# Kernel tuning notes

Hardware: AMD Instinct MI355X
Metric: run time of the kernel (lower is better)

Reference implementation:

```python
import jax, jax.numpy as jnp
import numpy as np

NH = 4096
OBS = 4096
OUT = 4096
T = 16


def _rk4_last(f, h0, t):
    """Fixed-step RK4 odeint over grid t; returns state at t[-1]."""
    def step(h, ts):
        t0, t1 = ts
        dt = t1 - t0
        half = dt * 0.5
        k1 = f(t0, h)
        k2 = f(t0 + half, h + half * k1)
        k3 = f(t0 + half, h + half * k2)
        k4 = f(t1, h + dt * k3)
        return h + (dt / 6.0) * (k1 + 2.0 * k2 + 2.0 * k3 + k4), None
    hT, _ = jax.lax.scan(step, h0, (t[:-1], t[1:]))
    return hT


def setup_inputs() -> dict:
    key = jax.random.key(0)
    ks = jax.random.split(key, 12)
    s = 0.02
    return {
        "x_f": jax.random.normal(ks[0], (1, OBS), jnp.float32),
        "x_b": jax.random.normal(ks[1], (1, OBS), jnp.float32),
        "h_f": jax.random.normal(ks[2], (NH,), jnp.float32),
        "h_b": jax.random.normal(ks[3], (NH,), jnp.float32),
        "t_f": jnp.linspace(0.0, 1.0, T, dtype=jnp.float32),
        "t_b": jnp.linspace(1.0, 0.0, T, dtype=jnp.float32),
        "i2h_W": jax.random.normal(ks[4], (NH, OBS + NH), jnp.float32) * s,
        "i2h_b": jax.random.normal(ks[5], (NH,), jnp.float32) * s,
        "h2o_W": jax.random.normal(ks[6], (OUT, 2 * NH), jnp.float32) * s,
        "h2o_b": jax.random.normal(ks[7], (OUT,), jnp.float32) * s,
        "f_W1": jax.random.normal(ks[8], (NH, NH), jnp.float32) * s,
        "f_b1": jax.random.normal(ks[9], (NH,), jnp.float32) * s,
        "f_W2": jax.random.normal(ks[10], (NH, NH), jnp.float32) * s,
        "f_b2": jax.random.normal(ks[11], (NH,), jnp.float32) * s,
    }


def reference(x_f, x_b, h_f, h_b, t_f, t_b,
              i2h_W, i2h_b, h2o_W, h2o_b, f_W1, f_b1, f_W2, f_b2):
    def func(t, h):  # ODE dynamics: 2-layer tanh MLP (time-independent)
        return f_W2 @ jnp.tanh(f_W1 @ h + f_b1) + f_b2

    def i2h(v):
        return i2h_W @ v + i2h_b

    def gru_update(x, h):
        # NOTE: original computes z and r from the SAME linear on the same
        # input, so z == r; we keep that math faithfully.
        g = jax.nn.sigmoid(i2h(jnp.concatenate([x, h])))
        z, r = g, g
        h_hat = jnp.tanh(i2h(jnp.concatenate([x, r * h])))
        return z * h + (1.0 - z) * h_hat

    h_f = _rk4_last(func, h_f, t_f)
    h_b = _rk4_last(func, h_b, t_b)

    h_f = gru_update(x_f[0], h_f)  # x_f.squeeze(0)
    h_b = gru_update(x_b[0], h_b)

    out = h2o_W @ jnp.concatenate([h_f, h_b]) + h2o_b
    return out, h_f, h_b
```

## Files before the change

kernel.cpp:

```cpp
#include <hip/hip_runtime.h>
#include <math.h>

#define NH   4096
#define KCAT 8192
#define TPTS 16

typedef unsigned short ushort_t;

__device__ __forceinline__ float wave_reduce64(float s) {
#pragma unroll
    for (int off = 32; off > 0; off >>= 1)
        s += __shfl_down(s, off, 64);
    return s;
}

__device__ __forceinline__ unsigned f2bf_pack2(float lo, float hi) {
    unsigned ul = __float_as_uint(lo);
    unsigned uh = __float_as_uint(hi);
    ul = (ul + 0x7fffu + ((ul >> 16) & 1u)) >> 16;
    uh = (uh + 0x7fffu + ((uh >> 16) & 1u)) >> 16;
    return ul | (uh << 16);
}

__device__ __forceinline__ ushort_t bf16_1(float x) {
    unsigned u = __float_as_uint(x);
    return (ushort_t)((u + 0x7fffu + ((u >> 16) & 1u)) >> 16);
}

__device__ __forceinline__ void bf16x8_to_f32(uint4 w, float* f) {
    f[0] = __uint_as_float(w.x << 16); f[1] = __uint_as_float(w.x & 0xffff0000u);
    f[2] = __uint_as_float(w.y << 16); f[3] = __uint_as_float(w.y & 0xffff0000u);
    f[4] = __uint_as_float(w.z << 16); f[5] = __uint_as_float(w.z & 0xffff0000u);
    f[6] = __uint_as_float(w.w << 16); f[7] = __uint_as_float(w.w & 0xffff0000u);
}

__global__ __launch_bounds__(256) void cvt_bf16_kernel(const float* __restrict__ src,
                                                       ushort_t* __restrict__ dst, int n8) {
    int i = blockIdx.x * 256 + threadIdx.x;
    if (i < n8) {
        const float4* s4 = (const float4*)src;
        float4 a = s4[2 * i], b = s4[2 * i + 1];
        uint4 o;
        o.x = f2bf_pack2(a.x, a.y);
        o.y = f2bf_pack2(a.z, a.w);
        o.z = f2bf_pack2(b.x, b.y);
        o.w = f2bf_pack2(b.z, b.w);
        ((uint4*)dst)[i] = o;
    }
}

__global__ __launch_bounds__(256) void init_hu(const float* __restrict__ h_f,
                                               const float* __restrict__ h_b,
                                               float* __restrict__ H,
                                               ushort_t* __restrict__ Ubf) {
    int i = blockIdx.x * 256 + threadIdx.x;
    float a = h_f[i], b = h_b[i];
    H[i]       = a;  H[NH + i]   = b;
    Ubf[i]     = bf16_1(a);
    Ubf[NH + i] = bf16_1(b);
}


__global__ __launch_bounds__(512, 4) void ode_mv1(
    const ushort_t* __restrict__ W1b, const float* __restrict__ b1,
    const ushort_t* __restrict__ Ubf, ushort_t* __restrict__ Vbf)
{
    __shared__ uint4 uS[1024];
    const int t = threadIdx.x;
    {
        const uint4* U4 = (const uint4*)Ubf;
        uS[t]       = U4[t];
        uS[t + 512] = U4[t + 512];
    }
    __syncthreads();

    const int l   = t & 63;
    const int row = blockIdx.x * 8 + (t >> 6);
    const uint4* __restrict__ W4 = (const uint4*)(W1b + (size_t)row * NH);

    float s0 = 0.f, s1 = 0.f;
#pragma unroll
    for (int i = 0; i < 8; ++i) {
        int idx = l + 64 * i;
        uint4 wv = W4[idx];
        uint4 u0 = uS[idx];
        uint4 u1 = uS[512 + idx];
        float wf[8], a0[8], a1[8];
        bf16x8_to_f32(wv, wf);
        bf16x8_to_f32(u0, a0);
        bf16x8_to_f32(u1, a1);
#pragma unroll
        for (int k = 0; k < 8; ++k) {
            s0 += wf[k] * a0[k];
            s1 += wf[k] * a1[k];
        }
    }
    s0 = wave_reduce64(s0);
    s1 = wave_reduce64(s1);
    if (l == 0) {
        float bb = b1[row];
        Vbf[row]      = bf16_1(tanhf(s0 + bb));
        Vbf[NH + row] = bf16_1(tanhf(s1 + bb));
    }
}

__global__ __launch_bounds__(512, 4) void ode_mv2(
    const ushort_t* __restrict__ W2b, const float* __restrict__ b2,
    const ushort_t* __restrict__ Vbf,
    const float* __restrict__ tf, const float* __restrict__ tb, int sidx,
    float wgt, float cnext, int stage,
    float* __restrict__ H, float* __restrict__ ACC,
    ushort_t* __restrict__ Ubf)
{
    __shared__ uint4 vS[1024];
    const int t = threadIdx.x;
    {
        const uint4* V4 = (const uint4*)Vbf;
        vS[t]       = V4[t];
        vS[t + 512] = V4[t + 512];
    }
    __syncthreads();

    const int l   = t & 63;
    const int row = blockIdx.x * 8 + (t >> 6);
    const uint4* __restrict__ W4 = (const uint4*)(W2b + (size_t)row * NH);
    const float dt0 = tf[sidx + 1] - tf[sidx];
    const float dt1 = tb[sidx + 1] - tb[sidx];

    float s0 = 0.f, s1 = 0.f;
#pragma unroll
    for (int i = 0; i < 8; ++i) {
        int idx = l + 64 * i;
        uint4 wv = W4[idx];
        uint4 v0 = vS[idx];
        uint4 v1 = vS[512 + idx];
        float wf[8], a0[8], a1[8];
        bf16x8_to_f32(wv, wf);
        bf16x8_to_f32(v0, a0);
        bf16x8_to_f32(v1, a1);
#pragma unroll
        for (int k = 0; k < 8; ++k) {
            s0 += wf[k] * a0[k];
            s1 += wf[k] * a1[k];
        }
    }
    s0 = wave_reduce64(s0);
    s1 = wave_reduce64(s1);
    if (l == 0) {
        float bb = b2[row];
        float k0 = s0 + bb, k1 = s1 + bb;
        float base0 = (stage == 0) ? H[row]      : ACC[row];
        float base1 = (stage == 0) ? H[NH + row] : ACC[NH + row];
        float a0 = base0 + wgt * (dt0 / 6.f) * k0;
        float a1 = base1 + wgt * (dt1 / 6.f) * k1;
        ACC[row]      = a0;
        ACC[NH + row] = a1;
        if (stage == 3) {
            H[row]      = a0;
            H[NH + row] = a1;
            Ubf[row]      = bf16_1(a0);
            Ubf[NH + row] = bf16_1(a1);
        } else {
            Ubf[row]      = bf16_1(H[row]      + cnext * dt0 * k0);
            Ubf[NH + row] = bf16_1(H[NH + row] + cnext * dt1 * k1);
        }
    }
}

__global__ __launch_bounds__(256) void init_h_kernel(const float* __restrict__ h_f,
                                                     const float* __restrict__ h_b,
                                                     float* __restrict__ H) {
    int i = blockIdx.x * 256 + threadIdx.x;
    H[i]      = h_f[i];
    H[NH + i] = h_b[i];
}

__global__ __launch_bounds__(256) void rk4_mv1_f32(
    const float* __restrict__ W1, const float* __restrict__ b1,
    const float* __restrict__ H,  const float* __restrict__ Kv,
    const float* __restrict__ tf, const float* __restrict__ tb,
    int tidx, float coef, int useK,
    float* __restrict__ V)
{
    const int row  = blockIdx.x * 4 + (threadIdx.x >> 6);
    const int lane = threadIdx.x & 63;
    const float a0 = coef * (tf[tidx + 1] - tf[tidx]);
    const float a1 = coef * (tb[tidx + 1] - tb[tidx]);

    const float4* __restrict__ W4 = (const float4*)(W1 + (size_t)row * NH);
    const float4* __restrict__ x0 = (const float4*)(H);
    const float4* __restrict__ x1 = (const float4*)(H + NH);
    const float4* __restrict__ k0 = (const float4*)(Kv);
    const float4* __restrict__ k1 = (const float4*)(Kv + NH);

    float s0 = 0.f, s1 = 0.f;
    if (useK) {
#pragma unroll 8
        for (int i = 0; i < NH / 4 / 64; ++i) {
            int idx = lane + i * 64;
            float4 w  = W4[idx];
            float4 h0 = x0[idx], h1 = x1[idx];
            float4 p0 = k0[idx], p1 = k1[idx];
            s0 += w.x * (h0.x + a0 * p0.x) + w.y * (h0.y + a0 * p0.y)
                + w.z * (h0.z + a0 * p0.z) + w.w * (h0.w + a0 * p0.w);
            s1 += w.x * (h1.x + a1 * p1.x) + w.y * (h1.y + a1 * p1.y)
                + w.z * (h1.z + a1 * p1.z) + w.w * (h1.w + a1 * p1.w);
        }
    } else {
#pragma unroll 8
        for (int i = 0; i < NH / 4 / 64; ++i) {
            int idx = lane + i * 64;
            float4 w  = W4[idx];
            float4 h0 = x0[idx], h1 = x1[idx];
            s0 += w.x * h0.x + w.y * h0.y + w.z * h0.z + w.w * h0.w;
            s1 += w.x * h1.x + w.y * h1.y + w.z * h1.z + w.w * h1.w;
        }
    }
    s0 = wave_reduce64(s0);
    s1 = wave_reduce64(s1);
    if (lane == 0) {
        float bb = b1[row];
        V[row]      = tanhf(s0 + bb);
        V[NH + row] = tanhf(s1 + bb);
    }
}

__global__ __launch_bounds__(256) void rk4_mv2_f32(
    const float* __restrict__ W2, const float* __restrict__ b2,
    const float* __restrict__ V,
    const float* __restrict__ tf, const float* __restrict__ tb,
    int tidx, float wgt,
    const float* __restrict__ Hbase,
    float* __restrict__ Kout, float* __restrict__ ACC)
{
    const int row  = blockIdx.x * 4 + (threadIdx.x >> 6);
    const int lane = threadIdx.x & 63;

    const float4* __restrict__ W4 = (const float4*)(W2 + (size_t)row * NH);
    const float4* __restrict__ v0 = (const float4*)(V);
    const float4* __restrict__ v1 = (const float4*)(V + NH);

    float s0 = 0.f, s1 = 0.f;
#pragma unroll 8
    for (int i = 0; i < NH / 4 / 64; ++i) {
        int idx = lane + i * 64;
        float4 w = W4[idx];
        float4 a = v0[idx], b = v1[idx];
        s0 += w.x * a.x + w.y * a.y + w.z * a.z + w.w * a.w;
        s1 += w.x * b.x + w.y * b.y + w.z * b.z + w.w * b.w;
    }
    s0 = wave_reduce64(s0);
    s1 = wave_reduce64(s1);
    if (lane == 0) {
        float bb  = b2[row];
        float k0v = s0 + bb;
        float k1v = s1 + bb;
        Kout[row]      = k0v;
        Kout[NH + row] = k1v;
        const float dt0 = tf[tidx + 1] - tf[tidx];
        const float dt1 = tb[tidx + 1] - tb[tidx];
        ACC[row]      = Hbase[row]      + wgt * (dt0 / 6.f) * k0v;
        ACC[NH + row] = Hbase[NH + row] + wgt * (dt1 / 6.f) * k1v;
    }
}

__global__ __launch_bounds__(256) void build_xcat_kernel(
    const float* __restrict__ x_f, const float* __restrict__ x_b,
    const float* __restrict__ H,
    float* __restrict__ xcat1, float* __restrict__ xcat2)
{
    int i = blockIdx.x * 256 + threadIdx.x;
    float xf = x_f[i], xb = x_b[i];
    xcat1[i]               = xf;
    xcat2[i]               = xf;
    xcat1[KCAT + i]        = xb;
    xcat2[KCAT + i]        = xb;
    xcat1[NH + i]          = H[i];
    xcat1[KCAT + NH + i]   = H[NH + i];
}

__global__ __launch_bounds__(256) void gru_mv1(
    const float* __restrict__ Wi, const float* __restrict__ bi,
    const float* __restrict__ xcat1, const float* __restrict__ H,
    float* __restrict__ G, float* __restrict__ xcat2)
{
    const int row  = blockIdx.x * 4 + (threadIdx.x >> 6);
    const int lane = threadIdx.x & 63;

    const float4* __restrict__ W4 = (const float4*)(Wi + (size_t)row * KCAT);
    const float4* __restrict__ c0 = (const float4*)(xcat1);
    const float4* __restrict__ c1 = (const float4*)(xcat1 + KCAT);

    float s0 = 0.f, s1 = 0.f;
#pragma unroll 8
    for (int i = 0; i < KCAT / 4 / 64; ++i) {
        int idx = lane + i * 64;
        float4 w = W4[idx];
        float4 a = c0[idx], b = c1[idx];
        s0 += w.x * a.x + w.y * a.y + w.z * a.z + w.w * a.w;
        s1 += w.x * b.x + w.y * b.y + w.z * b.z + w.w * b.w;
    }
    s0 = wave_reduce64(s0);
    s1 = wave_reduce64(s1);
    if (lane == 0) {
        float bb = bi[row];
        float g0 = 1.f / (1.f + expf(-(s0 + bb)));
        float g1 = 1.f / (1.f + expf(-(s1 + bb)));
        G[row]      = g0;
        G[NH + row] = g1;
        xcat2[NH + row]        = g0 * H[row];
        xcat2[KCAT + NH + row] = g1 * H[NH + row];
    }
}

__global__ __launch_bounds__(256) void gru_mv2(
    const float* __restrict__ Wi, const float* __restrict__ bi,
    const float* __restrict__ xcat2, const float* __restrict__ H,
    const float* __restrict__ G,
    float* __restrict__ out, float* __restrict__ hcat)
{
    const int row  = blockIdx.x * 4 + (threadIdx.x >> 6);
    const int lane = threadIdx.x & 63;

    const float4* __restrict__ W4 = (const float4*)(Wi + (size_t)row * KCAT);
    const float4* __restrict__ c0 = (const float4*)(xcat2);
    const float4* __restrict__ c1 = (const float4*)(xcat2 + KCAT);

    float s0 = 0.f, s1 = 0.f;
#pragma unroll 8
    for (int i = 0; i < KCAT / 4 / 64; ++i) {
        int idx = lane + i * 64;
        float4 w = W4[idx];
        float4 a = c0[idx], b = c1[idx];
        s0 += w.x * a.x + w.y * a.y + w.z * a.z + w.w * a.w;
        s1 += w.x * b.x + w.y * b.y + w.z * b.z + w.w * b.w;
    }
    s0 = wave_reduce64(s0);
    s1 = wave_reduce64(s1);
    if (lane == 0) {
        float bb  = bi[row];
        float hh0 = tanhf(s0 + bb);
        float hh1 = tanhf(s1 + bb);
        float g0  = G[row], g1 = G[NH + row];
        float hf  = g0 * H[row]      + (1.f - g0) * hh0;
        float hb  = g1 * H[NH + row] + (1.f - g1) * hh1;
        out[NH + row]     = hf;
        out[2 * NH + row] = hb;
        hcat[row]      = hf;
        hcat[NH + row] = hb;
    }
}

__global__ __launch_bounds__(256) void h2o_mv(
    const float* __restrict__ W, const float* __restrict__ b,
    const float* __restrict__ hcat, float* __restrict__ out)
{
    const int row  = blockIdx.x * 4 + (threadIdx.x >> 6);
    const int lane = threadIdx.x & 63;

    const float4* __restrict__ W4 = (const float4*)(W + (size_t)row * KCAT);
    const float4* __restrict__ x4 = (const float4*)(hcat);

    float s = 0.f;
#pragma unroll 8
    for (int i = 0; i < KCAT / 4 / 64; ++i) {
        int idx = lane + i * 64;
        float4 w = W4[idx];
        float4 a = x4[idx];
        s += w.x * a.x + w.y * a.y + w.z * a.z + w.w * a.w;
    }
    s = wave_reduce64(s);
    if (lane == 0)
        out[row] = s + b[row];
}

extern "C" void kernel_launch(void* const* d_in, const int* in_sizes, int n_in,
                              void* d_out, int out_size, void* d_ws, size_t ws_size,
                              hipStream_t stream) {
    const float* x_f   = (const float*)d_in[0];
    const float* x_b   = (const float*)d_in[1];
    const float* h_f   = (const float*)d_in[2];
    const float* h_b   = (const float*)d_in[3];
    const float* t_f   = (const float*)d_in[4];
    const float* t_b   = (const float*)d_in[5];
    const float* i2h_W = (const float*)d_in[6];
    const float* i2h_b = (const float*)d_in[7];
    const float* h2o_W = (const float*)d_in[8];
    const float* h2o_b = (const float*)d_in[9];
    const float* f_W1  = (const float*)d_in[10];
    const float* f_b1  = (const float*)d_in[11];
    const float* f_W2  = (const float*)d_in[12];
    const float* f_b2  = (const float*)d_in[13];
    float* out = (float*)d_out;

    float* ws    = (float*)d_ws;
    float* Hg    = ws;
    float* ACCg  = Hg    + 2 * NH;
    float* Vg32  = ACCg  + 2 * NH;
    float* Kg32  = Vg32  + 2 * NH;
    float* xcat1 = Kg32  + 2 * NH;
    float* xcat2 = xcat1 + 2 * KCAT;
    float* G     = xcat2 + 2 * KCAT;
    float* hcat  = G     + 2 * NH;
    float* fend  = hcat  + KCAT;
    ushort_t* Ubf = (ushort_t*)fend;
    ushort_t* Vbf = Ubf + 2 * NH;
    ushort_t* W1b = Vbf + 2 * NH;
    ushort_t* W2b = W1b + (size_t)NH * NH;
    size_t need = (size_t)((char*)(W2b + (size_t)NH * NH) - (char*)d_ws);
    const bool fast = ws_size >= need;

    dim3 blk(256);

    if (fast) {
        const int n8 = NH * NH / 8;
        cvt_bf16_kernel<<<n8 / 256, blk, 0, stream>>>(f_W1, W1b, n8);
        cvt_bf16_kernel<<<n8 / 256, blk, 0, stream>>>(f_W2, W2b, n8);
        init_hu<<<NH / 256, blk, 0, stream>>>(h_f, h_b, Hg, Ubf);

        for (int s = 0; s < TPTS - 1; ++s) {
            ode_mv1<<<512, 512, 0, stream>>>(W1b, f_b1, Ubf, Vbf);
            ode_mv2<<<512, 512, 0, stream>>>(W2b, f_b2, Vbf, t_f, t_b, s,
                                             1.f, 0.5f, 0, Hg, ACCg, Ubf);
            ode_mv1<<<512, 512, 0, stream>>>(W1b, f_b1, Ubf, Vbf);
            ode_mv2<<<512, 512, 0, stream>>>(W2b, f_b2, Vbf, t_f, t_b, s,
                                             2.f, 0.5f, 1, Hg, ACCg, Ubf);
            ode_mv1<<<512, 512, 0, stream>>>(W1b, f_b1, Ubf, Vbf);
            ode_mv2<<<512, 512, 0, stream>>>(W2b, f_b2, Vbf, t_f, t_b, s,
                                             2.f, 1.0f, 2, Hg, ACCg, Ubf);
            ode_mv1<<<512, 512, 0, stream>>>(W1b, f_b1, Ubf, Vbf);
            ode_mv2<<<512, 512, 0, stream>>>(W2b, f_b2, Vbf, t_f, t_b, s,
                                             1.f, 0.0f, 3, Hg, ACCg, Ubf);
        }
    } else {
        const int mv_grid = NH / 4;
        init_h_kernel<<<NH / 256, blk, 0, stream>>>(h_f, h_b, Hg);
        float* H   = Hg;
        float* ACC = ACCg;
        for (int s = 0; s < TPTS - 1; ++s) {
            rk4_mv1_f32<<<mv_grid, blk, 0, stream>>>(f_W1, f_b1, H, Kg32, t_f, t_b, s, 0.0f, 0, Vg32);
            rk4_mv2_f32<<<mv_grid, blk, 0, stream>>>(f_W2, f_b2, Vg32, t_f, t_b, s, 1.0f, H,   Kg32, ACC);
            rk4_mv1_f32<<<mv_grid, blk, 0, stream>>>(f_W1, f_b1, H, Kg32, t_f, t_b, s, 0.5f, 1, Vg32);
            rk4_mv2_f32<<<mv_grid, blk, 0, stream>>>(f_W2, f_b2, Vg32, t_f, t_b, s, 2.0f, ACC, Kg32, ACC);
            rk4_mv1_f32<<<mv_grid, blk, 0, stream>>>(f_W1, f_b1, H, Kg32, t_f, t_b, s, 0.5f, 1, Vg32);
            rk4_mv2_f32<<<mv_grid, blk, 0, stream>>>(f_W2, f_b2, Vg32, t_f, t_b, s, 2.0f, ACC, Kg32, ACC);
            rk4_mv1_f32<<<mv_grid, blk, 0, stream>>>(f_W1, f_b1, H, Kg32, t_f, t_b, s, 1.0f, 1, Vg32);
            rk4_mv2_f32<<<mv_grid, blk, 0, stream>>>(f_W2, f_b2, Vg32, t_f, t_b, s, 1.0f, ACC, Kg32, ACC);
            float* tmp = H; H = ACC; ACC = tmp;
        }
        if (H != Hg) {
            hipMemcpyAsync(Hg, H, 2 * NH * sizeof(float), hipMemcpyDeviceToDevice, stream);
        }
    }

    const int mv_grid = NH / 4;
    build_xcat_kernel<<<NH / 256, blk, 0, stream>>>(x_f, x_b, Hg, xcat1, xcat2);
    gru_mv1<<<mv_grid, blk, 0, stream>>>(i2h_W, i2h_b, xcat1, Hg, G, xcat2);
    gru_mv2<<<mv_grid, blk, 0, stream>>>(i2h_W, i2h_b, xcat2, Hg, G, out, hcat);
    h2o_mv <<<mv_grid, blk, 0, stream>>>(h2o_W, h2o_b, hcat, out);
}
```

Measured before the change: 1.328 ms.

## Run RK4 ODE loop in a persistent cooperative kernel with register-resident weights

```diff
diff --git a/kernel.cpp b/kernel.cpp
--- a/kernel.cpp
+++ b/kernel.cpp
@@ -4,6 +4,7 @@
 #define NH   4096
 #define KCAT 8192
 #define TPTS 16
+#define NBLK 256
 
 typedef unsigned short ushort_t;
 
@@ -11,6 +12,13 @@
 #pragma unroll
     for (int off = 32; off > 0; off >>= 1)
         s += __shfl_down(s, off, 64);
+    return s;
+}
+
+__device__ __forceinline__ float wrx64(float s) {
+#pragma unroll
+    for (int off = 32; off > 0; off >>= 1)
+        s += __shfl_xor(s, off, 64);
     return s;
 }
 
@@ -33,6 +41,172 @@
     f[4] = __uint_as_float(w.z << 16); f[5] = __uint_as_float(w.z & 0xffff0000u);
     f[6] = __uint_as_float(w.w << 16); f[7] = __uint_as_float(w.w & 0xffff0000u);
 }
+
+
+__device__ __forceinline__ void grid_barrier(unsigned* bar) {
+    __syncthreads();
+    if (threadIdx.x == 0) {
+        unsigned* leaf = bar + 32 * (blockIdx.x >> 4);
+        unsigned* root = bar + 32 * 16;
+        unsigned* gen  = bar + 32 * 17;
+        unsigned g = __hip_atomic_load(gen, __ATOMIC_RELAXED, __HIP_MEMORY_SCOPE_AGENT);
+        bool done = false;
+        if (__hip_atomic_fetch_add(leaf, 1u, __ATOMIC_ACQ_REL, __HIP_MEMORY_SCOPE_AGENT) == 15u) {
+            __hip_atomic_store(leaf, 0u, __ATOMIC_RELAXED, __HIP_MEMORY_SCOPE_AGENT);
+            if (__hip_atomic_fetch_add(root, 1u, __ATOMIC_ACQ_REL, __HIP_MEMORY_SCOPE_AGENT) == 15u) {
+                __hip_atomic_store(root, 0u, __ATOMIC_RELAXED, __HIP_MEMORY_SCOPE_AGENT);
+                __hip_atomic_store(gen, g + 1u, __ATOMIC_RELEASE, __HIP_MEMORY_SCOPE_AGENT);
+                done = true;
+            }
+        }
+        if (!done) {
+            while (__hip_atomic_load(gen, __ATOMIC_ACQUIRE, __HIP_MEMORY_SCOPE_AGENT) == g)
+                __builtin_amdgcn_s_sleep(2);
+        }
+    }
+    __syncthreads();
+}
+
+__global__ __launch_bounds__(64) void zero_bar(unsigned* bar) {
+    for (int i = threadIdx.x; i < 1024; i += 64) bar[i] = 0;
+}
+
+#define MV_DOT(WA, WB)                                                        \
+    {                                                                         \
+        s00 = 0.f; s01 = 0.f; s10 = 0.f; s11 = 0.f;                           \
+        _Pragma("unroll")                                                     \
+        for (int k = 0; k < 32; ++k) {                                        \
+            float4 uu = *(const float4*)&uS[4 * l + 256 * k];                 \
+            float wA0 = __uint_as_float(WA[k] << 16);                         \
+            float wA1 = __uint_as_float(WA[k] & 0xffff0000u);                 \
+            float wB0 = __uint_as_float(WB[k] << 16);                         \
+            float wB1 = __uint_as_float(WB[k] & 0xffff0000u);                 \
+            s00 = fmaf(wA0, uu.x, s00); s01 = fmaf(wA0, uu.y, s01);           \
+            s00 = fmaf(wA1, uu.z, s00); s01 = fmaf(wA1, uu.w, s01);           \
+            s10 = fmaf(wB0, uu.x, s10); s11 = fmaf(wB0, uu.y, s11);           \
+            s10 = fmaf(wB1, uu.z, s10); s11 = fmaf(wB1, uu.w, s11);           \
+        }                                                                     \
+        s00 = wrx64(s00); s01 = wrx64(s01);                                   \
+        s10 = wrx64(s10); s11 = wrx64(s11);                                   \
+    }
+
+#define STAGE_U(SRCP)                                                         \
+    {                                                                         \
+        const float4* g4_ = (const float4*)(SRCP);                            \
+        float4* d4_ = (float4*)uS;                                            \
+        _Pragma("unroll")                                                     \
+        for (int i_ = 0; i_ < 4; ++i_)                                        \
+            d4_[t + 512 * i_] = g4_[t + 512 * i_];                            \
+    }
+
+__global__ __launch_bounds__(512, 2) void ode_persistent(
+    const float* __restrict__ W1, const float* __restrict__ b1,
+    const float* __restrict__ W2, const float* __restrict__ b2,
+    const float* __restrict__ h_f, const float* __restrict__ h_b,
+    const float* __restrict__ tf, const float* __restrict__ tb,
+    float2* __restrict__ Ug2, float2* __restrict__ Vg2,
+    unsigned* __restrict__ bar, float* __restrict__ Hg)
+{
+    __shared__ float uS[2 * NH];
+    const int t  = threadIdx.x;
+    const int l  = t & 63;
+    const int w  = t >> 6;
+    const int r0 = blockIdx.x * 16 + 2 * w;
+    const int r1 = r0 + 1;
+
+    unsigned w1a[32], w1b[32], w2a[32], w2b[32];
+    {
+        const float2* p0 = (const float2*)(W1 + (size_t)r0 * NH);
+        const float2* p1 = (const float2*)(W1 + (size_t)r1 * NH);
+        const float2* q0 = (const float2*)(W2 + (size_t)r0 * NH);
+        const float2* q1 = (const float2*)(W2 + (size_t)r1 * NH);
+#pragma unroll
+        for (int k = 0; k < 32; ++k) {
+            int idx = l + 64 * k;
+            float2 a = p0[idx];
+            float2 b = p1[idx];
+            float2 c = q0[idx];
+            float2 d = q1[idx];
+            w1a[k] = f2bf_pack2(a.x, a.y);
+            w1b[k] = f2bf_pack2(b.x, b.y);
+            w2a[k] = f2bf_pack2(c.x, c.y);
+            w2b[k] = f2bf_pack2(d.x, d.y);
+        }
+    }
+
+    {
+        const float4* hf4 = (const float4*)h_f;
+        const float4* hb4 = (const float4*)h_b;
+        float4* d4 = (float4*)uS;
+#pragma unroll
+        for (int i = 0; i < 2; ++i) {
+            float4 a = hf4[t + 512 * i];
+            float4 b = hb4[t + 512 * i];
+            d4[2 * (t + 512 * i)]     = make_float4(a.x, b.x, a.y, b.y);
+            d4[2 * (t + 512 * i) + 1] = make_float4(a.z, b.z, a.w, b.w);
+        }
+    }
+
+    float H00 = h_f[r0], H01 = h_b[r0], H10 = h_f[r1], H11 = h_b[r1];
+    const float bb10 = b1[r0], bb11 = b1[r1];
+    const float bb20 = b2[r0], bb21 = b2[r1];
+    float A00 = 0.f, A01 = 0.f, A10 = 0.f, A11 = 0.f;
+
+    __syncthreads();
+
+    for (int s = 0; s < TPTS - 1; ++s) {
+        const float dt0 = tf[s + 1] - tf[s];
+        const float dt1 = tb[s + 1] - tb[s];
+        for (int st = 0; st < 4; ++st) {
+            float s00, s01, s10, s11;
+
+            MV_DOT(w1a, w1b);
+            {
+                float v00 = tanhf(s00 + bb10), v01 = tanhf(s01 + bb10);
+                float v10 = tanhf(s10 + bb11), v11 = tanhf(s11 + bb11);
+                if (l == 0) {
+                    Vg2[r0] = make_float2(v00, v01);
+                    Vg2[r1] = make_float2(v10, v11);
+                }
+            }
+            grid_barrier(bar);
+            STAGE_U(Vg2);
+            __syncthreads();
+
+            MV_DOT(w2a, w2b);
+            {
+                float k00 = s00 + bb20, k01 = s01 + bb20;
+                float k10 = s10 + bb21, k11 = s11 + bb21;
+                float wgt = (st == 1 || st == 2) ? 2.f : 1.f;
+                if (st == 0) { A00 = H00; A01 = H01; A10 = H10; A11 = H11; }
+                A00 += wgt * (dt0 / 6.f) * k00;  A01 += wgt * (dt1 / 6.f) * k01;
+                A10 += wgt * (dt0 / 6.f) * k10;  A11 += wgt * (dt1 / 6.f) * k11;
+                float u00, u01, u10, u11;
+                if (st == 3) {
+                    H00 = A00; H01 = A01; H10 = A10; H11 = A11;
+                    u00 = H00; u01 = H01; u10 = H10; u11 = H11;
+                } else {
+                    float cn = (st == 2) ? 1.f : 0.5f;
+                    u00 = H00 + cn * dt0 * k00;  u01 = H01 + cn * dt1 * k01;
+                    u10 = H10 + cn * dt0 * k10;  u11 = H11 + cn * dt1 * k11;
+                }
+                if (l == 0) {
+                    Ug2[r0] = make_float2(u00, u01);
+                    Ug2[r1] = make_float2(u10, u11);
+                }
+            }
+            grid_barrier(bar);
+            STAGE_U(Ug2);
+            __syncthreads();
+        }
+    }
+
+    if (l == 0) {
+        Hg[r0]      = H00;  Hg[NH + r0] = H01;
+        Hg[r1]      = H10;  Hg[NH + r1] = H11;
+    }
+}
+
 
 __global__ __launch_bounds__(256) void cvt_bf16_kernel(const float* __restrict__ src,
                                                        ushort_t* __restrict__ dst, int n8) {
@@ -59,7 +233,6 @@
     Ubf[i]     = bf16_1(a);
     Ubf[NH + i] = bf16_1(b);
 }
-
 
 __global__ __launch_bounds__(512, 4) void ode_mv1(
     const ushort_t* __restrict__ W1b, const float* __restrict__ b1,
@@ -410,46 +583,64 @@
     size_t need = (size_t)((char*)(W2b + (size_t)NH * NH) - (char*)d_ws);
     const bool fast = ws_size >= need;
 
+    float2*   Ug2  = (float2*)W1b;
+    float2*   Vg2  = Ug2 + NH;
+    unsigned* barp = (unsigned*)(Vg2 + NH);
+    size_t coop_need = (size_t)((char*)(barp + 1024) - (char*)d_ws);
+
     dim3 blk(256);
 
-    if (fast) {
-        const int n8 = NH * NH / 8;
-        cvt_bf16_kernel<<<n8 / 256, blk, 0, stream>>>(f_W1, W1b, n8);
-        cvt_bf16_kernel<<<n8 / 256, blk, 0, stream>>>(f_W2, W2b, n8);
-        init_hu<<<NH / 256, blk, 0, stream>>>(h_f, h_b, Hg, Ubf);
-
-        for (int s = 0; s < TPTS - 1; ++s) {
-            ode_mv1<<<512, 512, 0, stream>>>(W1b, f_b1, Ubf, Vbf);
-            ode_mv2<<<512, 512, 0, stream>>>(W2b, f_b2, Vbf, t_f, t_b, s,
-                                             1.f, 0.5f, 0, Hg, ACCg, Ubf);
-            ode_mv1<<<512, 512, 0, stream>>>(W1b, f_b1, Ubf, Vbf);
-            ode_mv2<<<512, 512, 0, stream>>>(W2b, f_b2, Vbf, t_f, t_b, s,
-                                             2.f, 0.5f, 1, Hg, ACCg, Ubf);
-            ode_mv1<<<512, 512, 0, stream>>>(W1b, f_b1, Ubf, Vbf);
-            ode_mv2<<<512, 512, 0, stream>>>(W2b, f_b2, Vbf, t_f, t_b, s,
-                                             2.f, 1.0f, 2, Hg, ACCg, Ubf);
-            ode_mv1<<<512, 512, 0, stream>>>(W1b, f_b1, Ubf, Vbf);
-            ode_mv2<<<512, 512, 0, stream>>>(W2b, f_b2, Vbf, t_f, t_b, s,
-                                             1.f, 0.0f, 3, Hg, ACCg, Ubf);
-        }
-    } else {
-        const int mv_grid = NH / 4;
-        init_h_kernel<<<NH / 256, blk, 0, stream>>>(h_f, h_b, Hg);
-        float* H   = Hg;
-        float* ACC = ACCg;
-        for (int s = 0; s < TPTS - 1; ++s) {
-            rk4_mv1_f32<<<mv_grid, blk, 0, stream>>>(f_W1, f_b1, H, Kg32, t_f, t_b, s, 0.0f, 0, Vg32);
-            rk4_mv2_f32<<<mv_grid, blk, 0, stream>>>(f_W2, f_b2, Vg32, t_f, t_b, s, 1.0f, H,   Kg32, ACC);
-            rk4_mv1_f32<<<mv_grid, blk, 0, stream>>>(f_W1, f_b1, H, Kg32, t_f, t_b, s, 0.5f, 1, Vg32);
-            rk4_mv2_f32<<<mv_grid, blk, 0, stream>>>(f_W2, f_b2, Vg32, t_f, t_b, s, 2.0f, ACC, Kg32, ACC);
-            rk4_mv1_f32<<<mv_grid, blk, 0, stream>>>(f_W1, f_b1, H, Kg32, t_f, t_b, s, 0.5f, 1, Vg32);
-            rk4_mv2_f32<<<mv_grid, blk, 0, stream>>>(f_W2, f_b2, Vg32, t_f, t_b, s, 2.0f, ACC, Kg32, ACC);
-            rk4_mv1_f32<<<mv_grid, blk, 0, stream>>>(f_W1, f_b1, H, Kg32, t_f, t_b, s, 1.0f, 1, Vg32);
-            rk4_mv2_f32<<<mv_grid, blk, 0, stream>>>(f_W2, f_b2, Vg32, t_f, t_b, s, 1.0f, ACC, Kg32, ACC);
-            float* tmp = H; H = ACC; ACC = tmp;
-        }
-        if (H != Hg) {
-            hipMemcpyAsync(Hg, H, 2 * NH * sizeof(float), hipMemcpyDeviceToDevice, stream);
+    bool ode_done = false;
+    if (ws_size >= coop_need) {
+        zero_bar<<<1, 64, 0, stream>>>(barp);
+        void* kargs[] = { (void*)&f_W1, (void*)&f_b1, (void*)&f_W2, (void*)&f_b2,
+                          (void*)&h_f,  (void*)&h_b,  (void*)&t_f,  (void*)&t_b,
+                          (void*)&Ug2,  (void*)&Vg2,  (void*)&barp, (void*)&Hg };
+        hipError_t e = hipLaunchCooperativeKernel(ode_persistent, dim3(NBLK), dim3(512),
+                                                  kargs, 0, stream);
+        ode_done = (e == hipSuccess);
+    }
+
+    if (!ode_done) {
+        if (fast) {
+            const int n8 = NH * NH / 8;
+            cvt_bf16_kernel<<<n8 / 256, blk, 0, stream>>>(f_W1, W1b, n8);
+            cvt_bf16_kernel<<<n8 / 256, blk, 0, stream>>>(f_W2, W2b, n8);
+            init_hu<<<NH / 256, blk, 0, stream>>>(h_f, h_b, Hg, Ubf);
+
+            for (int s = 0; s < TPTS - 1; ++s) {
+                ode_mv1<<<512, 512, 0, stream>>>(W1b, f_b1, Ubf, Vbf);
+                ode_mv2<<<512, 512, 0, stream>>>(W2b, f_b2, Vbf, t_f, t_b, s,
+                                                 1.f, 0.5f, 0, Hg, ACCg, Ubf);
+                ode_mv1<<<512, 512, 0, stream>>>(W1b, f_b1, Ubf, Vbf);
+                ode_mv2<<<512, 512, 0, stream>>>(W2b, f_b2, Vbf, t_f, t_b, s,
+                                                 2.f, 0.5f, 1, Hg, ACCg, Ubf);
+                ode_mv1<<<512, 512, 0, stream>>>(W1b, f_b1, Ubf, Vbf);
+                ode_mv2<<<512, 512, 0, stream>>>(W2b, f_b2, Vbf, t_f, t_b, s,
+                                                 2.f, 1.0f, 2, Hg, ACCg, Ubf);
+                ode_mv1<<<512, 512, 0, stream>>>(W1b, f_b1, Ubf, Vbf);
+                ode_mv2<<<512, 512, 0, stream>>>(W2b, f_b2, Vbf, t_f, t_b, s,
+                                                 1.f, 0.0f, 3, Hg, ACCg, Ubf);
+            }
+        } else {
+            const int mv_grid = NH / 4;
+            init_h_kernel<<<NH / 256, blk, 0, stream>>>(h_f, h_b, Hg);
+            float* H   = Hg;
+            float* ACC = ACCg;
+            for (int s = 0; s < TPTS - 1; ++s) {
+                rk4_mv1_f32<<<mv_grid, blk, 0, stream>>>(f_W1, f_b1, H, Kg32, t_f, t_b, s, 0.0f, 0, Vg32);
+                rk4_mv2_f32<<<mv_grid, blk, 0, stream>>>(f_W2, f_b2, Vg32, t_f, t_b, s, 1.0f, H,   Kg32, ACC);
+                rk4_mv1_f32<<<mv_grid, blk, 0, stream>>>(f_W1, f_b1, H, Kg32, t_f, t_b, s, 0.5f, 1, Vg32);
+                rk4_mv2_f32<<<mv_grid, blk, 0, stream>>>(f_W2, f_b2, Vg32, t_f, t_b, s, 2.0f, ACC, Kg32, ACC);
+                rk4_mv1_f32<<<mv_grid, blk, 0, stream>>>(f_W1, f_b1, H, Kg32, t_f, t_b, s, 0.5f, 1, Vg32);
+                rk4_mv2_f32<<<mv_grid, blk, 0, stream>>>(f_W2, f_b2, Vg32, t_f, t_b, s, 2.0f, ACC, Kg32, ACC);
+                rk4_mv1_f32<<<mv_grid, blk, 0, stream>>>(f_W1, f_b1, H, Kg32, t_f, t_b, s, 1.0f, 1, Vg32);
+                rk4_mv2_f32<<<mv_grid, blk, 0, stream>>>(f_W2, f_b2, Vg32, t_f, t_b, s, 1.0f, ACC, Kg32, ACC);
+                float* tmp = H; H = ACC; ACC = tmp;
+            }
+            if (H != Hg) {
+                hipMemcpyAsync(Hg, H, 2 * NH * sizeof(float), hipMemcpyDeviceToDevice, stream);
+            }
         }
     }
 
```

After: 3.444 ms. 2.59x slower.

## Replace per-stage ODE launches with persistent cooperative kernel holding weights in registers

Applied to the files above, without the earlier changes.

```diff
diff --git a/kernel.cpp b/kernel.cpp
--- a/kernel.cpp
+++ b/kernel.cpp
@@ -4,6 +4,7 @@
 #define NH   4096
 #define KCAT 8192
 #define TPTS 16
+#define NBLK 256
 
 typedef unsigned short ushort_t;
 
@@ -33,6 +34,156 @@
     f[4] = __uint_as_float(w.z << 16); f[5] = __uint_as_float(w.z & 0xffff0000u);
     f[6] = __uint_as_float(w.w << 16); f[7] = __uint_as_float(w.w & 0xffff0000u);
 }
+
+
+__device__ __forceinline__ void grid_barrier(unsigned* bar) {
+    __syncthreads();
+    if (threadIdx.x == 0) {
+        unsigned* leaf = bar + 32 * (blockIdx.x >> 4);
+        unsigned* root = bar + 32 * 16;
+        unsigned* gen  = bar + 32 * 17;
+        unsigned g = __hip_atomic_load(gen, __ATOMIC_RELAXED, __HIP_MEMORY_SCOPE_AGENT);
+        bool done = false;
+        if (__hip_atomic_fetch_add(leaf, 1u, __ATOMIC_ACQ_REL, __HIP_MEMORY_SCOPE_AGENT) == 15u) {
+            __hip_atomic_store(leaf, 0u, __ATOMIC_RELAXED, __HIP_MEMORY_SCOPE_AGENT);
+            if (__hip_atomic_fetch_add(root, 1u, __ATOMIC_ACQ_REL, __HIP_MEMORY_SCOPE_AGENT) == 15u) {
+                __hip_atomic_store(root, 0u, __ATOMIC_RELAXED, __HIP_MEMORY_SCOPE_AGENT);
+                __hip_atomic_store(gen, g + 1u, __ATOMIC_RELEASE, __HIP_MEMORY_SCOPE_AGENT);
+                done = true;
+            }
+        }
+        if (!done) {
+            while (__hip_atomic_load(gen, __ATOMIC_ACQUIRE, __HIP_MEMORY_SCOPE_AGENT) == g)
+                __builtin_amdgcn_s_sleep(2);
+        }
+    }
+    __syncthreads();
+}
+
+__global__ __launch_bounds__(64) void zero_bar(unsigned* bar) {
+    for (int i = threadIdx.x; i < 1024; i += 64) bar[i] = 0;
+}
+
+#define REP32(X) X(0) X(1) X(2) X(3) X(4) X(5) X(6) X(7) \
+                 X(8) X(9) X(10) X(11) X(12) X(13) X(14) X(15) \
+                 X(16) X(17) X(18) X(19) X(20) X(21) X(22) X(23) \
+                 X(24) X(25) X(26) X(27) X(28) X(29) X(30) X(31)
+
+#define DECL_W(K)  unsigned w1_##K, w2_##K;
+
+#define LOAD_W(K)  { float2 a_ = p0[l + 64 * K]; float2 c_ = q0[l + 64 * K]; \
+                     w1_##K = f2bf_pack2(a_.x, a_.y);                        \
+                     w2_##K = f2bf_pack2(c_.x, c_.y); }
+
+#define DOT_1(K)   { uint2 uu_ = *(const uint2*)(uB + 128 * K);              \
+                     float a0_ = __uint_as_float(uu_.x << 16);               \
+                     float a1_ = __uint_as_float(uu_.x & 0xffff0000u);       \
+                     float c0_ = __uint_as_float(uu_.y << 16);               \
+                     float c1_ = __uint_as_float(uu_.y & 0xffff0000u);       \
+                     float lo_ = __uint_as_float(w1_##K << 16);              \
+                     float hi_ = __uint_as_float(w1_##K & 0xffff0000u);      \
+                     s0 = fmaf(lo_, a0_, s0); s1 = fmaf(lo_, a1_, s1);       \
+                     s0 = fmaf(hi_, c0_, s0); s1 = fmaf(hi_, c1_, s1); }
+
+#define DOT_2(K)   { uint2 uu_ = *(const uint2*)(uB + 128 * K);              \
+                     float a0_ = __uint_as_float(uu_.x << 16);               \
+                     float a1_ = __uint_as_float(uu_.x & 0xffff0000u);       \
+                     float c0_ = __uint_as_float(uu_.y << 16);               \
+                     float c1_ = __uint_as_float(uu_.y & 0xffff0000u);       \
+                     float lo_ = __uint_as_float(w2_##K << 16);              \
+                     float hi_ = __uint_as_float(w2_##K & 0xffff0000u);      \
+                     s0 = fmaf(lo_, a0_, s0); s1 = fmaf(lo_, a1_, s1);       \
+                     s0 = fmaf(hi_, c0_, s0); s1 = fmaf(hi_, c1_, s1); }
+
+__global__ __launch_bounds__(1024, 4) void ode_persistent(
+    const float* __restrict__ W1, const float* __restrict__ b1,
+    const float* __restrict__ W2, const float* __restrict__ b2,
+    const float* __restrict__ h_f, const float* __restrict__ h_b,
+    const float* __restrict__ tf, const float* __restrict__ tb,
+    unsigned* __restrict__ Ugu, unsigned* __restrict__ Vgu,
+    unsigned* __restrict__ bar, float* __restrict__ Hg)
+{
+    __shared__ unsigned uS[NH];
+    const int t   = threadIdx.x;
+    const int l   = t & 63;
+    const int w   = t >> 6;
+    const int row = blockIdx.x * 16 + w;
+
+    REP32(DECL_W)
+    {
+        const float2* p0 = (const float2*)(W1 + (size_t)row * NH);
+        const float2* q0 = (const float2*)(W2 + (size_t)row * NH);
+        REP32(LOAD_W)
+    }
+
+    {
+        const float4* hf4 = (const float4*)h_f;
+        const float4* hb4 = (const float4*)h_b;
+        float4 a = hf4[t];
+        float4 b = hb4[t];
+        uint4 o;
+        o.x = f2bf_pack2(a.x, b.x);
+        o.y = f2bf_pack2(a.y, b.y);
+        o.z = f2bf_pack2(a.z, b.z);
+        o.w = f2bf_pack2(a.w, b.w);
+        ((uint4*)uS)[t] = o;
+    }
+
+    float H0 = h_f[row], H1 = h_b[row];
+    const float bb1 = b1[row];
+    const float bb2 = b2[row];
+    float A0 = 0.f, A1 = 0.f;
+    const unsigned* uB = uS + 2 * l;
+
+    __syncthreads();
+
+    for (int s = 0; s < TPTS - 1; ++s) {
+        const float dt0 = tf[s + 1] - tf[s];
+        const float dt1 = tb[s + 1] - tb[s];
+        for (int st = 0; st < 4; ++st) {
+            float s0, s1;
+
+            s0 = 0.f; s1 = 0.f;
+            REP32(DOT_1)
+            s0 = wave_reduce64(s0); s1 = wave_reduce64(s1);
+            if (l == 0)
+                Vgu[row] = f2bf_pack2(tanhf(s0 + bb1), tanhf(s1 + bb1));
+            grid_barrier(bar);
+            ((uint4*)uS)[t] = ((const uint4*)Vgu)[t];
+            __syncthreads();
+
+            s0 = 0.f; s1 = 0.f;
+            REP32(DOT_2)
+            s0 = wave_reduce64(s0); s1 = wave_reduce64(s1);
+            {
+                float k0 = s0 + bb2, k1 = s1 + bb2;
+                float wgt = (st == 1 || st == 2) ? 2.f : 1.f;
+                if (st == 0) { A0 = H0; A1 = H1; }
+                A0 += wgt * (dt0 / 6.f) * k0;
+                A1 += wgt * (dt1 / 6.f) * k1;
+                float u0, u1;
+                if (st == 3) {
+                    H0 = A0; H1 = A1;
+                    u0 = H0; u1 = H1;
+                } else {
+                    float cn = (st == 2) ? 1.f : 0.5f;
+                    u0 = H0 + cn * dt0 * k0;
+                    u1 = H1 + cn * dt1 * k1;
+                }
+                if (l == 0) Ugu[row] = f2bf_pack2(u0, u1);
+            }
+            grid_barrier(bar);
+            ((uint4*)uS)[t] = ((const uint4*)Ugu)[t];
+            __syncthreads();
+        }
+    }
+
+    if (l == 0) {
+        Hg[row]      = H0;
+        Hg[NH + row] = H1;
+    }
+}
+
 
 __global__ __launch_bounds__(256) void cvt_bf16_kernel(const float* __restrict__ src,
                                                        ushort_t* __restrict__ dst, int n8) {
@@ -59,7 +210,6 @@
     Ubf[i]     = bf16_1(a);
     Ubf[NH + i] = bf16_1(b);
 }
-
 
 __global__ __launch_bounds__(512, 4) void ode_mv1(
     const ushort_t* __restrict__ W1b, const float* __restrict__ b1,
@@ -410,46 +560,64 @@
     size_t need = (size_t)((char*)(W2b + (size_t)NH * NH) - (char*)d_ws);
     const bool fast = ws_size >= need;
 
+    unsigned* Ugu  = (unsigned*)W1b;
+    unsigned* Vgu  = Ugu + NH;
+    unsigned* barp = Vgu + NH;
+    size_t coop_need = (size_t)((char*)(barp + 1024) - (char*)d_ws);
+
     dim3 blk(256);
 
-    if (fast) {
-        const int n8 = NH * NH / 8;
-        cvt_bf16_kernel<<<n8 / 256, blk, 0, stream>>>(f_W1, W1b, n8);
-        cvt_bf16_kernel<<<n8 / 256, blk, 0, stream>>>(f_W2, W2b, n8);
-        init_hu<<<NH / 256, blk, 0, stream>>>(h_f, h_b, Hg, Ubf);
-
-        for (int s = 0; s < TPTS - 1; ++s) {
-            ode_mv1<<<512, 512, 0, stream>>>(W1b, f_b1, Ubf, Vbf);
-            ode_mv2<<<512, 512, 0, stream>>>(W2b, f_b2, Vbf, t_f, t_b, s,
-                                             1.f, 0.5f, 0, Hg, ACCg, Ubf);
-            ode_mv1<<<512, 512, 0, stream>>>(W1b, f_b1, Ubf, Vbf);
-            ode_mv2<<<512, 512, 0, stream>>>(W2b, f_b2, Vbf, t_f, t_b, s,
-                                             2.f, 0.5f, 1, Hg, ACCg, Ubf);
-            ode_mv1<<<512, 512, 0, stream>>>(W1b, f_b1, Ubf, Vbf);
-            ode_mv2<<<512, 512, 0, stream>>>(W2b, f_b2, Vbf, t_f, t_b, s,
-                                             2.f, 1.0f, 2, Hg, ACCg, Ubf);
-            ode_mv1<<<512, 512, 0, stream>>>(W1b, f_b1, Ubf, Vbf);
-            ode_mv2<<<512, 512, 0, stream>>>(W2b, f_b2, Vbf, t_f, t_b, s,
-                                             1.f, 0.0f, 3, Hg, ACCg, Ubf);
-        }
-    } else {
-        const int mv_grid = NH / 4;
-        init_h_kernel<<<NH / 256, blk, 0, stream>>>(h_f, h_b, Hg);
-        float* H   = Hg;
-        float* ACC = ACCg;
-        for (int s = 0; s < TPTS - 1; ++s) {
-            rk4_mv1_f32<<<mv_grid, blk, 0, stream>>>(f_W1, f_b1, H, Kg32, t_f, t_b, s, 0.0f, 0, Vg32);
-            rk4_mv2_f32<<<mv_grid, blk, 0, stream>>>(f_W2, f_b2, Vg32, t_f, t_b, s, 1.0f, H,   Kg32, ACC);
-            rk4_mv1_f32<<<mv_grid, blk, 0, stream>>>(f_W1, f_b1, H, Kg32, t_f, t_b, s, 0.5f, 1, Vg32);
-            rk4_mv2_f32<<<mv_grid, blk, 0, stream>>>(f_W2, f_b2, Vg32, t_f, t_b, s, 2.0f, ACC, Kg32, ACC);
-            rk4_mv1_f32<<<mv_grid, blk, 0, stream>>>(f_W1, f_b1, H, Kg32, t_f, t_b, s, 0.5f, 1, Vg32);
-            rk4_mv2_f32<<<mv_grid, blk, 0, stream>>>(f_W2, f_b2, Vg32, t_f, t_b, s, 2.0f, ACC, Kg32, ACC);
-            rk4_mv1_f32<<<mv_grid, blk, 0, stream>>>(f_W1, f_b1, H, Kg32, t_f, t_b, s, 1.0f, 1, Vg32);
-            rk4_mv2_f32<<<mv_grid, blk, 0, stream>>>(f_W2, f_b2, Vg32, t_f, t_b, s, 1.0f, ACC, Kg32, ACC);
-            float* tmp = H; H = ACC; ACC = tmp;
-        }
-        if (H != Hg) {
-            hipMemcpyAsync(Hg, H, 2 * NH * sizeof(float), hipMemcpyDeviceToDevice, stream);
+    bool ode_done = false;
+    if (ws_size >= coop_need) {
+        zero_bar<<<1, 64, 0, stream>>>(barp);
+        void* kargs[] = { (void*)&f_W1, (void*)&f_b1, (void*)&f_W2, (void*)&f_b2,
+                          (void*)&h_f,  (void*)&h_b,  (void*)&t_f,  (void*)&t_b,
+                          (void*)&Ugu,  (void*)&Vgu,  (void*)&barp, (void*)&Hg };
+        hipError_t e = hipLaunchCooperativeKernel(ode_persistent, dim3(NBLK), dim3(1024),
+                                                  kargs, 0, stream);
+        ode_done = (e == hipSuccess);
+    }
+
+    if (!ode_done) {
+        if (fast) {
+            const int n8 = NH * NH / 8;
+            cvt_bf16_kernel<<<n8 / 256, blk, 0, stream>>>(f_W1, W1b, n8);
+            cvt_bf16_kernel<<<n8 / 256, blk, 0, stream>>>(f_W2, W2b, n8);
+            init_hu<<<NH / 256, blk, 0, stream>>>(h_f, h_b, Hg, Ubf);
+
+            for (int s = 0; s < TPTS - 1; ++s) {
+                ode_mv1<<<512, 512, 0, stream>>>(W1b, f_b1, Ubf, Vbf);
+                ode_mv2<<<512, 512, 0, stream>>>(W2b, f_b2, Vbf, t_f, t_b, s,
+                                                 1.f, 0.5f, 0, Hg, ACCg, Ubf);
+                ode_mv1<<<512, 512, 0, stream>>>(W1b, f_b1, Ubf, Vbf);
+                ode_mv2<<<512, 512, 0, stream>>>(W2b, f_b2, Vbf, t_f, t_b, s,
+                                                 2.f, 0.5f, 1, Hg, ACCg, Ubf);
+                ode_mv1<<<512, 512, 0, stream>>>(W1b, f_b1, Ubf, Vbf);
+                ode_mv2<<<512, 512, 0, stream>>>(W2b, f_b2, Vbf, t_f, t_b, s,
+                                                 2.f, 1.0f, 2, Hg, ACCg, Ubf);
+                ode_mv1<<<512, 512, 0, stream>>>(W1b, f_b1, Ubf, Vbf);
+                ode_mv2<<<512, 512, 0, stream>>>(W2b, f_b2, Vbf, t_f, t_b, s,
+                                                 1.f, 0.0f, 3, Hg, ACCg, Ubf);
+            }
+        } else {
+            const int mv_grid = NH / 4;
+            init_h_kernel<<<NH / 256, blk, 0, stream>>>(h_f, h_b, Hg);
+            float* H   = Hg;
+            float* ACC = ACCg;
+            for (int s = 0; s < TPTS - 1; ++s) {
+                rk4_mv1_f32<<<mv_grid, blk, 0, stream>>>(f_W1, f_b1, H, Kg32, t_f, t_b, s, 0.0f, 0, Vg32);
+                rk4_mv2_f32<<<mv_grid, blk, 0, stream>>>(f_W2, f_b2, Vg32, t_f, t_b, s, 1.0f, H,   Kg32, ACC);
+                rk4_mv1_f32<<<mv_grid, blk, 0, stream>>>(f_W1, f_b1, H, Kg32, t_f, t_b, s, 0.5f, 1, Vg32);
+                rk4_mv2_f32<<<mv_grid, blk, 0, stream>>>(f_W2, f_b2, Vg32, t_f, t_b, s, 2.0f, ACC, Kg32, ACC);
+                rk4_mv1_f32<<<mv_grid, blk, 0, stream>>>(f_W1, f_b1, H, Kg32, t_f, t_b, s, 0.5f, 1, Vg32);
+                rk4_mv2_f32<<<mv_grid, blk, 0, stream>>>(f_W2, f_b2, Vg32, t_f, t_b, s, 2.0f, ACC, Kg32, ACC);
+                rk4_mv1_f32<<<mv_grid, blk, 0, stream>>>(f_W1, f_b1, H, Kg32, t_f, t_b, s, 1.0f, 1, Vg32);
+                rk4_mv2_f32<<<mv_grid, blk, 0, stream>>>(f_W2, f_b2, Vg32, t_f, t_b, s, 1.0f, ACC, Kg32, ACC);
+                float* tmp = H; H = ACC; ACC = tmp;
+            }
+            if (H != Hg) {
+                hipMemcpyAsync(Hg, H, 2 * NH * sizeof(float), hipMemcpyDeviceToDevice, stream);
+            }
         }
     }
 
```

After: 4.478 ms. +237.2%, slower.
